# Kernel tuning notes

Hardware: AMD Instinct MI355X
Metric: run time of the kernel (lower is better)

Reference implementation:

```python
import jax, jax.numpy as jnp
import numpy as np

# kernel hyperparameters (base_params)
NUGGET = 0.001
REG_LAMBDA = 0.01
FIT_L, FIT_SIGMA = 1.0, 1.0
MMD_L, MMD_SIGMA = 1.0, 1.0
N, D = 4096, 4


def rbf_gram(X1, X2, l, sigma):
    # [N1,N2] radial kernel: sigma^2 * exp(-||x-x'||^2 / (2 l^2)), vectorized
    sq = (jnp.sum(X1 * X1, axis=1)[:, None]
          + jnp.sum(X2 * X2, axis=1)[None, :]
          - 2.0 * (X1 @ X2.T))
    sq = jnp.maximum(sq, 0.0)
    return (sigma * sigma) * jnp.exp(-sq / (2.0 * l * l))


def setup_inputs() -> dict:
    key = jax.random.key(0)
    kx, ky, kz = jax.random.split(key, 3)
    X = jax.random.normal(kx, (N, D), dtype=jnp.float32)
    Y = jax.random.normal(ky, (N, D), dtype=jnp.float32)
    Z = Y + 0.1 * jax.random.normal(kz, (N, D), dtype=jnp.float32)  # Z init'd from Y, perturbed
    return {"X": X, "Y": Y, "Z": Z}


def reference(X, Y, Z):
    # fit_kXX and its nugget-regularized inverse (precomputed in __init__)
    fit_kXX = rbf_gram(X, X, FIT_L, FIT_SIGMA)
    fit_kXX_inv = jnp.linalg.inv(fit_kXX + NUGGET * jnp.eye(X.shape[0], dtype=X.dtype))

    # loss_fit_z: ||k_ZZ||_F^2 - 2 ||k_ZY||_F^2  (torch matrix norm = Frobenius)
    k_ZZ = rbf_gram(Z, Z, MMD_L, MMD_SIGMA)
    k_ZY = rbf_gram(Z, Y, MMD_L, MMD_SIGMA)
    loss_fit = jnp.sum(k_ZZ * k_ZZ) - 2.0 * jnp.sum(k_ZY * k_ZY)

    # loss_reg_z: reg_lambda * trace(Z^T fit_kXX_inv Z)
    loss_reg = REG_LAMBDA * jnp.sum(Z * (fit_kXX_inv @ Z))

    return loss_fit + loss_reg
```

## Files before the change

### kernel.cpp

```cpp
#include <hip/hip_runtime.h>


#define NN 4096
#define LDA 4100
#define OFF_W   ((size_t)NN*LDA)
#define OFF_ACC (OFF_W + (size_t)NN*4)

__device__ __forceinline__ float rdlane(float v, int l){
    return __int_as_float(__builtin_amdgcn_readlane(__float_as_int(v), l));
}

__device__ void wave_chol64(const float* Dm, float* __restrict__ A, int h){
    const int lane = threadIdx.x & 63;
    float row[64];
#pragma unroll
    for (int q=0;q<16;q++){
        float4 v = *(const float4*)(Dm + lane*68 + q*4);
        row[q*4]=v.x; row[q*4+1]=v.y; row[q*4+2]=v.z; row[q*4+3]=v.w;
    }
#pragma unroll
    for (int j=0;j<64;j++){
        float d  = rdlane(row[j], j);
        float sd = sqrtf(d);
        float inv= 1.0f/sd;
        float v  = (lane==j)? sd : row[j]*inv;
        row[j] = v;
#pragma unroll
        for (int c=j+1;c<64;c++){
            float lc = rdlane(v, c);
            row[c] -= v*lc;
        }
    }
#pragma unroll
    for (int q=0;q<16;q++)
        *(float4*)(A + (size_t)(h+lane)*LDA + h + q*4) =
            make_float4(row[q*4],row[q*4+1],row[q*4+2],row[q*4+3]);
}

__global__ void k_build_A(const float* __restrict__ X, float* __restrict__ A){
    const int i  = blockIdx.y;
    const int j0 = (blockIdx.x*256 + threadIdx.x)*4;
    const float4 xi = *(const float4*)(X + (size_t)i*4);
    float out[4];
#pragma unroll
    for (int s=0;s<4;s++){
        const float4 xj = *(const float4*)(X + (size_t)(j0+s)*4);
        float d0=xi.x-xj.x, d1=xi.y-xj.y, d2=xi.z-xj.z, d3=xi.w-xj.w;
        float sq = d0*d0+d1*d1+d2*d2+d3*d3;
        float v  = __expf(-0.5f*sq);
        if (i == j0+s) v += 0.001f;
        out[s]=v;
    }
    *(float4*)(A + (size_t)i*LDA + j0) = make_float4(out[0],out[1],out[2],out[3]);
}

__global__ void k_init(const float* __restrict__ Z, float* __restrict__ W,
                       double* __restrict__ acc){
    const int i = blockIdx.x*256+threadIdx.x;
    ((float4*)W)[i] = ((const float4*)Z)[i];
    if (blockIdx.x==0 && threadIdx.x==0) acc[0]=0.0;
}

__global__ __launch_bounds__(256) void k_chol0(float* __restrict__ A){
    __shared__ float Dm[64*68];
    const int tid = threadIdx.x;
#pragma unroll
    for (int it=0; it<4; ++it){
        int idx = tid + it*256, r = idx>>4, q = idx&15;
        float4 v = *(const float4*)(A + (size_t)r*LDA + q*4);
        *(float4*)&Dm[r*68 + q*4] = v;
    }
    __syncthreads();
    if (tid < 64) wave_chol64(Dm, A, 0);
}

__global__ __launch_bounds__(256) void k_trsm2(float* __restrict__ A, float* __restrict__ W,
                                               int g){
    __shared__ float Ld[64*68];
    __shared__ float dinv[64];
    const int tid = threadIdx.x;
    const int s0  = g*64;
#pragma unroll
    for (int it=0; it<4; ++it){
        int idx = tid + it*256, r = idx>>4, q = idx&15;
        float4 v = *(const float4*)(A + (size_t)(s0+r)*LDA + s0 + q*4);
        *(float4*)&Ld[r*68 + q*4] = v;
    }
    __syncthreads();
    if (tid < 64) dinv[tid] = 1.0f/Ld[tid*68 + tid];
    __syncthreads();

    const int nRB = (66-g)>>2;
    if ((int)blockIdx.x < nRB){
        const int row = s0 + 64 + blockIdx.x*256 + tid;
        const int rl  = row>4095 ? 4095 : row;
        float x[64];
        const float* src = A + (size_t)rl*LDA + s0;
#pragma unroll
        for (int q=0;q<16;q++){
            float4 v = *(const float4*)(src + q*4);
            x[q*4]=v.x; x[q*4+1]=v.y; x[q*4+2]=v.z; x[q*4+3]=v.w;
        }
#pragma unroll
        for (int c=0;c<64;c++){
            float xc = x[c]*dinv[c];
            x[c] = xc;
#pragma unroll
            for (int t=c+1;t<64;t++) x[t] -= xc*Ld[t*68 + c];
        }
        if (row < 4096){
            float* dst = A + (size_t)row*LDA + s0;
#pragma unroll
            for (int q=0;q<16;q++)
                *(float4*)(dst + q*4) = make_float4(x[q*4],x[q*4+1],x[q*4+2],x[q*4+3]);
        }
    } else {
        if (tid < 64){
            const int lane = tid;
            float4 wv = *(const float4*)(W + (size_t)(s0+lane)*4);
            float w0=wv.x, w1=wv.y, w2=wv.z, w3=wv.w;
#pragma unroll
            for (int j=0;j<64;j++){
                if (lane==j){ float dj=dinv[j]; w0*=dj; w1*=dj; w2*=dj; w3*=dj; }
                float b0=__shfl(w0,j), b1=__shfl(w1,j), b2=__shfl(w2,j), b3=__shfl(w3,j);
                float l = Ld[lane*68 + j];
                if (lane>j){ w0-=l*b0; w1-=l*b1; w2-=l*b2; w3-=l*b3; }
            }
            *(float4*)(W + (size_t)(s0+lane)*4) = make_float4(w0,w1,w2,w3);
        }
    }
}

__global__ __launch_bounds__(256) void k_pupd(float* __restrict__ A, float* __restrict__ W,
                                              int g){
    __shared__ float Sh[2*4352];
    const int tid = threadIdx.x;
    const int g64 = g*64;
    const int i = g&3, ncols = 3-i;
    int idx = blockIdx.x;
    int c_blk=-1, r_blk=-1;
#pragma unroll
    for (int cc=0; cc<3; ++cc){
        if (cc < ncols && c_blk < 0){
            int cb = g+1+cc, cnt = 64-cb;
            if (idx < cnt){ c_blk=cb; r_blk=cb+idx; }
            else idx -= cnt;
        }
    }
    const int tx = tid&15, ty = tid>>4;

    if (c_blk >= 0){
        float* PrT = Sh;
        float* PcT = (r_blk==c_blk) ? Sh : (Sh + 4352);
        const int r0 = r_blk*64, c0 = c_blk*64;
#pragma unroll
        for (int it=0; it<4; ++it){
            int ix = tid + it*256, r = ix>>4, q = ix&15;
            float4 v = *(const float4*)(A + (size_t)(r0+r)*LDA + g64 + q*4);
            PrT[(q*4+0)*68+r]=v.x; PrT[(q*4+1)*68+r]=v.y;
            PrT[(q*4+2)*68+r]=v.z; PrT[(q*4+3)*68+r]=v.w;
        }
        if (r_blk != c_blk){
#pragma unroll
            for (int it=0; it<4; ++it){
                int ix = tid + it*256, r = ix>>4, q = ix&15;
                float4 v = *(const float4*)(A + (size_t)(c0+r)*LDA + g64 + q*4);
                PcT[(q*4+0)*68+r]=v.x; PcT[(q*4+1)*68+r]=v.y;
                PcT[(q*4+2)*68+r]=v.z; PcT[(q*4+3)*68+r]=v.w;
            }
        }
        __syncthreads();
        float acc[4][4]={};
#pragma unroll 8
        for (int t=0;t<64;t++){
            float4 a = *(const float4*)&PrT[t*68 + ty*4];
            float4 b = *(const float4*)&PcT[t*68 + tx*4];
            acc[0][0]+=a.x*b.x; acc[0][1]+=a.x*b.y; acc[0][2]+=a.x*b.z; acc[0][3]+=a.x*b.w;
            acc[1][0]+=a.y*b.x; acc[1][1]+=a.y*b.y; acc[1][2]+=a.y*b.z; acc[1][3]+=a.y*b.w;
            acc[2][0]+=a.z*b.x; acc[2][1]+=a.z*b.y; acc[2][2]+=a.z*b.z; acc[2][3]+=a.z*b.w;
            acc[3][0]+=a.w*b.x; acc[3][1]+=a.w*b.y; acc[3][2]+=a.w*b.z; acc[3][3]+=a.w*b.w;
        }
        if (r_blk==c_blk && c_blk==g+1){
            float* Dm = Sh + 4352;
            __syncthreads();
#pragma unroll
            for (int ii=0;ii<4;ii++){
                float4 c = *(const float4*)(A + (size_t)(r0+ty*4+ii)*LDA + c0 + tx*4);
                c.x-=acc[ii][0]; c.y-=acc[ii][1]; c.z-=acc[ii][2]; c.w-=acc[ii][3];
                *(float4*)&Dm[(ty*4+ii)*68 + tx*4] = c;
            }
            __syncthreads();
            if (tid < 64) wave_chol64(Dm, A, r0);
        } else {
#pragma unroll
            for (int ii=0;ii<4;ii++){
                float* p = A + (size_t)(r0+ty*4+ii)*LDA + c0 + tx*4;
                float4 cv = *(float4*)p;
                cv.x-=acc[ii][0]; cv.y-=acc[ii][1]; cv.z-=acc[ii][2]; cv.w-=acc[ii][3];
                *(float4*)p = cv;
            }
        }
    } else {
        const int wr0 = (g+1+idx)*64;
        float* Lt = Sh;
        float* Ws = Sh + 4352;
#pragma unroll
        for (int it=0; it<4; ++it){
            int ix = tid + it*256, r = ix>>4, q = ix&15;
            float4 v = *(const float4*)(A + (size_t)(wr0+r)*LDA + g64 + q*4);
            *(float4*)&Lt[r*68 + q*4] = v;
        }
        if (tid < 64) *(float4*)&Ws[tid*4] = *(const float4*)(W + (size_t)(g64+tid)*4);
        __syncthreads();
        const int row = tid>>2, cw = tid&3;
        float s = 0.f;
#pragma unroll 16
        for (int t=0;t<64;t++) s += Lt[row*68+t]*Ws[t*4+cw];
        float* wp = W + (size_t)(wr0+row)*4 + cw;
        *wp = *wp - s;
    }
}

__global__ __launch_bounds__(256) void k_upd256(float* __restrict__ A, int S){
    __shared__ float S_[8704];
    const int tid = threadIdx.x;
    const int k0 = S*256, base = k0+256;
    const int T2 = (4096-base)>>7;
    const int nT2 = T2*(T2+1)/2;
    const int tx = tid&15, ty = tid>>4;

    if ((int)blockIdx.x == nT2){
        float* PT = S_;
        float* Dm = S_ + 4352;
        float acc[4][4]={};
        for (int kk=0; kk<4; ++kk){
            __syncthreads();
#pragma unroll
            for (int it=0; it<4; ++it){
                int ix = tid + it*256, r = ix>>4, q = ix&15;
                float4 v = *(const float4*)(A + (size_t)(base+r)*LDA + k0 + kk*64 + q*4);
                PT[(q*4+0)*68+r]=v.x; PT[(q*4+1)*68+r]=v.y;
                PT[(q*4+2)*68+r]=v.z; PT[(q*4+3)*68+r]=v.w;
            }
            __syncthreads();
#pragma unroll 8
            for (int t=0;t<64;t++){
                float4 a = *(const float4*)&PT[t*68 + ty*4];
                float4 b = *(const float4*)&PT[t*68 + tx*4];
                acc[0][0]+=a.x*b.x; acc[0][1]+=a.x*b.y; acc[0][2]+=a.x*b.z; acc[0][3]+=a.x*b.w;
                acc[1][0]+=a.y*b.x; acc[1][1]+=a.y*b.y; acc[1][2]+=a.y*b.z; acc[1][3]+=a.y*b.w;
                acc[2][0]+=a.z*b.x; acc[2][1]+=a.z*b.y; acc[2][2]+=a.z*b.z; acc[2][3]+=a.z*b.w;
                acc[3][0]+=a.w*b.x; acc[3][1]+=a.w*b.y; acc[3][2]+=a.w*b.z; acc[3][3]+=a.w*b.w;
            }
        }
        __syncthreads();
#pragma unroll
        for (int ii=0;ii<4;ii++){
            float4 c = *(const float4*)(A + (size_t)(base+ty*4+ii)*LDA + base + tx*4);
            c.x-=acc[ii][0]; c.y-=acc[ii][1]; c.z-=acc[ii][2]; c.w-=acc[ii][3];
            *(float4*)&Dm[(ty*4+ii)*68 + tx*4] = c;
        }
        __syncthreads();
        if (tid < 64) wave_chol64(Dm, A, base);
        return;
    }

    float* Sa = S_;
    float* Sb = S_ + 4224;
    int t2 = blockIdx.x;
    int bi = (int)((sqrtf(8.f*(float)t2+1.f)-1.f)*0.5f);
    while ((bi+1)*(bi+2)/2 <= t2) ++bi;
    while (bi*(bi+1)/2 > t2) --bi;
    const int bj = t2 - bi*(bi+1)/2;
    const int r0 = base + bi*128, c0 = base + bj*128;
    const bool dg = (bi==bj);
    const float* Sbp = dg ? Sa : Sb;
    int row_[4], q_[4];
#pragma unroll
    for (int it=0;it<4;++it){ int ix=tid+it*256; row_[it]=ix>>3; q_[it]=ix&7; }
    float4 ra[4], rb[4];
#pragma unroll
    for (int it=0;it<4;++it){
        ra[it] = *(const float4*)(A + (size_t)(r0+row_[it])*LDA + k0 + q_[it]*4);
        if (!dg) rb[it] = *(const float4*)(A + (size_t)(c0+row_[it])*LDA + k0 + q_[it]*4);
    }
    float acc[8][8]={};
    for (int kk=0;kk<8;++kk){
        __syncthreads();
#pragma unroll
        for (int it=0;it<4;++it){
            Sa[(q_[it]*4+0)*132+row_[it]]=ra[it].x; Sa[(q_[it]*4+1)*132+row_[it]]=ra[it].y;
            Sa[(q_[it]*4+2)*132+row_[it]]=ra[it].z; Sa[(q_[it]*4+3)*132+row_[it]]=ra[it].w;
            if (!dg){
                Sb[(q_[it]*4+0)*132+row_[it]]=rb[it].x; Sb[(q_[it]*4+1)*132+row_[it]]=rb[it].y;
                Sb[(q_[it]*4+2)*132+row_[it]]=rb[it].z; Sb[(q_[it]*4+3)*132+row_[it]]=rb[it].w;
            }
        }
        __syncthreads();
        if (kk < 7){
            const int kb = k0 + (kk+1)*32;
#pragma unroll
            for (int it=0;it<4;++it){
                ra[it] = *(const float4*)(A + (size_t)(r0+row_[it])*LDA + kb + q_[it]*4);
                if (!dg) rb[it] = *(const float4*)(A + (size_t)(c0+row_[it])*LDA + kb + q_[it]*4);
            }
        }
#pragma unroll 4
        for (int t=0;t<32;++t){
            float4 a0 = *(const float4*)&Sa[t*132 + ty*8];
            float4 a1 = *(const float4*)&Sa[t*132 + ty*8 + 4];
            float4 b0 = *(const float4*)&Sbp[t*132 + tx*8];
            float4 b1 = *(const float4*)&Sbp[t*132 + tx*8 + 4];
            float av[8]={a0.x,a0.y,a0.z,a0.w,a1.x,a1.y,a1.z,a1.w};
            float bv[8]={b0.x,b0.y,b0.z,b0.w,b1.x,b1.y,b1.z,b1.w};
#pragma unroll
            for (int ii=0;ii<8;ii++)
#pragma unroll
                for (int jj=0;jj<8;jj++) acc[ii][jj] += av[ii]*bv[jj];
        }
    }
#pragma unroll
    for (int ii=0;ii<8;ii++){
        const int r = r0 + ty*8 + ii;
        const int c = c0 + tx*8;
        if (r < base+64 && c < base+64) continue;
        float* p = A + (size_t)r*LDA + c;
        float4 c1 = *(float4*)p;
        c1.x-=acc[ii][0]; c1.y-=acc[ii][1]; c1.z-=acc[ii][2]; c1.w-=acc[ii][3];
        *(float4*)p = c1;
        float4 c2 = *(float4*)(p+4);
        c2.x-=acc[ii][4]; c2.y-=acc[ii][5]; c2.z-=acc[ii][6]; c2.w-=acc[ii][7];
        *(float4*)(p+4) = c2;
    }
}

__global__ void k_lossfit(const float* __restrict__ Z, const float* __restrict__ Y,
                          double* __restrict__ acc){
    const int tid=threadIdx.x;
    const int i0=blockIdx.x*8;
    double s=0.0;
    for (int ii=0;ii<8;ii++){
        const float4 zi = *(const float4*)(Z + (size_t)(i0+ii)*4);
        for (int j=tid;j<NN;j+=256){
            float4 zj = *(const float4*)(Z + (size_t)j*4);
            float4 yj = *(const float4*)(Y + (size_t)j*4);
            float d0=zi.x-zj.x, d1=zi.y-zj.y, d2=zi.z-zj.z, d3=zi.w-zj.w;
            float dzz = d0*d0+d1*d1+d2*d2+d3*d3;
            d0=zi.x-yj.x; d1=zi.y-yj.y; d2=zi.z-yj.z; d3=zi.w-yj.w;
            float dzy = d0*d0+d1*d1+d2*d2+d3*d3;
            s += (double)(__expf(-dzz) - 2.f*__expf(-dzy));
        }
    }
    for (int o=32;o;o>>=1) s += __shfl_down(s,o);
    __shared__ double ps[4];
    if ((tid&63)==0) ps[tid>>6]=s;
    __syncthreads();
    if (tid==0) atomicAdd(acc, ps[0]+ps[1]+ps[2]+ps[3]);
}

__global__ void k_finish(const float* __restrict__ W, const double* __restrict__ acc,
                         float* __restrict__ out){
    const int tid=threadIdx.x;
    double s=0.0;
    for (int r=tid;r<NN;r+=256){
        float4 v=*(const float4*)(W+(size_t)r*4);
        s += (double)v.x*v.x+(double)v.y*v.y+(double)v.z*v.z+(double)v.w*v.w;
    }
    for (int o=32;o;o>>=1) s += __shfl_down(s,o);
    __shared__ double ps[4];
    if ((tid&63)==0) ps[tid>>6]=s;
    __syncthreads();
    if (tid==0) out[0] = (float)(acc[0] + 0.01*(ps[0]+ps[1]+ps[2]+ps[3]));
}

extern "C" void kernel_launch(void* const* d_in, const int* in_sizes, int n_in,
                              void* d_out, int out_size, void* d_ws, size_t ws_size,
                              hipStream_t stream){
    const float* X=(const float*)d_in[0];
    const float* Y=(const float*)d_in[1];
    const float* Z=(const float*)d_in[2];
    float* ws   = (float*)d_ws;
    float* A    = ws;
    float* W    = ws + OFF_W;
    double* acc = (double*)(ws + OFF_ACC);

    if (ws_size < (OFF_ACC)*sizeof(float) + 16) return;

    k_init   <<<16,256,0,stream>>>(Z, W, acc);
    k_build_A<<<dim3(NN/1024,NN),256,0,stream>>>(X, A);
    k_lossfit<<<512,256,0,stream>>>(Z, Y, acc);
    k_chol0  <<<1,256,0,stream>>>(A);

    for (int g=0; g<64; ++g){
        const int nRB = (66-g)>>2;
        k_trsm2<<<nRB+1,256,0,stream>>>(A, W, g);
        const int i = g&3, ncols = 3-i;
        int ntile = 0;
        for (int cc=0; cc<ncols; ++cc) ntile += 64-(g+1+cc);
        const int nW = 63-g;
        if (ntile+nW > 0) k_pupd<<<ntile+nW,256,0,stream>>>(A, W, g);
        if (i==3 && g<63){
            const int S = g>>2;
            const int T2 = (4096-(S+1)*256)>>7;
            const int nT2 = T2*(T2+1)/2;
            k_upd256<<<nT2+1,256,0,stream>>>(A, S);
        }
    }
    k_finish<<<1,256,0,stream>>>(W, acc, (float*)d_out);
}
```

Baseline: 3.625 ms.

## Fuse panel TRSM, panel update and forward solve into one launch per step

Replaces the separate trsm and panel-update kernels with one fused kernel per 64-column step. In it, each update block recomputes its own TRSM rows from the diagonal block, the forward substitution on W is folded into the TRSM and Cholesky-solve paths, and the next diagonal block is factored in the same launch. Solved panel rows go to a compact 256-wide Lp buffer, which the 256-step trailing update reads instead of strided A rows. The aim is to halve the number of launches and serial dependencies along the critical path. The cost is redundant triangular solves in every update block, plus a B-tile layout change in the big update kernel.

Result: slower. 4.572 ms (+26.1%).

```diff
diff --git a/kernel.cpp b/kernel.cpp
--- a/kernel.cpp
+++ b/kernel.cpp
@@ -4,13 +4,15 @@
 #define NN 4096
 #define LDA 4100
 #define OFF_W   ((size_t)NN*LDA)
-#define OFF_ACC (OFF_W + (size_t)NN*4)
+#define OFF_LP  (OFF_W + (size_t)NN*4)
+#define OFF_ACC (OFF_LP + (size_t)4096*256)
 
 __device__ __forceinline__ float rdlane(float v, int l){
     return __int_as_float(__builtin_amdgcn_readlane(__float_as_int(v), l));
 }
 
-__device__ void wave_chol64(const float* Dm, float* __restrict__ A, int h){
+__device__ void wave_chol_solve(const float* Dm, float* __restrict__ A, int h,
+                                float4 w, float* __restrict__ W){
     const int lane = threadIdx.x & 63;
     float row[64];
 #pragma unroll
@@ -35,6 +37,15 @@
     for (int q=0;q<16;q++)
         *(float4*)(A + (size_t)(h+lane)*LDA + h + q*4) =
             make_float4(row[q*4],row[q*4+1],row[q*4+2],row[q*4+3]);
+    float w0=w.x,w1=w.y,w2=w.z,w3=w.w;
+#pragma unroll
+    for (int j=0;j<64;j++){
+        if (lane==j){ float dj=1.0f/row[j]; w0*=dj; w1*=dj; w2*=dj; w3*=dj; }
+        float b0=__shfl(w0,j), b1=__shfl(w1,j), b2=__shfl(w2,j), b3=__shfl(w3,j);
+        float l = row[j];
+        if (lane>j){ w0-=l*b0; w1-=l*b1; w2-=l*b2; w3-=l*b3; }
+    }
+    *(float4*)(W + (size_t)(h+lane)*4) = make_float4(w0,w1,w2,w3);
 }
 
 __global__ void k_build_A(const float* __restrict__ X, float* __restrict__ A){
@@ -61,41 +72,50 @@
     if (blockIdx.x==0 && threadIdx.x==0) acc[0]=0.0;
 }
 
-__global__ __launch_bounds__(256) void k_chol0(float* __restrict__ A){
+__global__ __launch_bounds__(256) void k_chol0(float* __restrict__ A, float* __restrict__ W){
     __shared__ float Dm[64*68];
+    const int tid=threadIdx.x;
+#pragma unroll
+    for (int it=0; it<4; ++it){
+        int idx=tid+it*256, r=idx>>4, q=idx&15;
+        *(float4*)&Dm[r*68+q*4] = *(const float4*)(A + (size_t)r*LDA + q*4);
+    }
+    __syncthreads();
+    if (tid<64){
+        float4 w = *(const float4*)(W + (size_t)tid*4);
+        wave_chol_solve(Dm, A, 0, w, W);
+    }
+}
+
+__global__ __launch_bounds__(256) void k_F(float* __restrict__ A, float* __restrict__ W,
+                                           float* __restrict__ Lp, int g){
+    __shared__ float S_[13376];
+    float* Ld   = S_;
+    float* dinv = S_+4352;
+    float* Wg   = S_+4416;
+    float* LrT  = S_+4672;
+    float* LcT  = S_+9024;
     const int tid = threadIdx.x;
-#pragma unroll
+    const int g64 = g*64;
+    const int pend = g|3;
+    const bool hasD = (g&3)!=3;
+    const int nT = (63-g+3)>>2;
+
     for (int it=0; it<4; ++it){
         int idx = tid + it*256, r = idx>>4, q = idx&15;
-        float4 v = *(const float4*)(A + (size_t)r*LDA + q*4);
-        *(float4*)&Dm[r*68 + q*4] = v;
-    }
+        *(float4*)&Ld[r*68+q*4] = *(const float4*)(A + (size_t)(g64+r)*LDA + g64 + q*4);
+    }
+    if (tid < 64) *(float4*)&Wg[tid*4] = *(const float4*)(W + (size_t)(g64+tid)*4);
     __syncthreads();
-    if (tid < 64) wave_chol64(Dm, A, 0);
-}
-
-__global__ __launch_bounds__(256) void k_trsm2(float* __restrict__ A, float* __restrict__ W,
-                                               int g){
-    __shared__ float Ld[64*68];
-    __shared__ float dinv[64];
-    const int tid = threadIdx.x;
-    const int s0  = g*64;
-#pragma unroll
-    for (int it=0; it<4; ++it){
-        int idx = tid + it*256, r = idx>>4, q = idx&15;
-        float4 v = *(const float4*)(A + (size_t)(s0+r)*LDA + s0 + q*4);
-        *(float4*)&Ld[r*68 + q*4] = v;
-    }
+    if (tid < 64) dinv[tid] = 1.0f/Ld[tid*68+tid];
     __syncthreads();
-    if (tid < 64) dinv[tid] = 1.0f/Ld[tid*68 + tid];
-    __syncthreads();
-
-    const int nRB = (66-g)>>2;
-    if ((int)blockIdx.x < nRB){
-        const int row = s0 + 64 + blockIdx.x*256 + tid;
+
+    int bid = blockIdx.x;
+    if (bid < nT){
+        const int row = g64 + 64 + bid*256 + tid;
         const int rl  = row>4095 ? 4095 : row;
         float x[64];
-        const float* src = A + (size_t)rl*LDA + s0;
+        const float* src = A + (size_t)rl*LDA + g64;
 #pragma unroll
         for (int q=0;q<16;q++){
             float4 v = *(const float4*)(src + q*4);
@@ -109,122 +129,143 @@
             for (int t=c+1;t<64;t++) x[t] -= xc*Ld[t*68 + c];
         }
         if (row < 4096){
-            float* dst = A + (size_t)row*LDA + s0;
+            float* lp = Lp + (size_t)row*256 + (g&3)*64;
 #pragma unroll
             for (int q=0;q<16;q++)
-                *(float4*)(dst + q*4) = make_float4(x[q*4],x[q*4+1],x[q*4+2],x[q*4+3]);
-        }
-    } else {
-        if (tid < 64){
-            const int lane = tid;
-            float4 wv = *(const float4*)(W + (size_t)(s0+lane)*4);
-            float w0=wv.x, w1=wv.y, w2=wv.z, w3=wv.w;
-#pragma unroll
-            for (int j=0;j<64;j++){
-                if (lane==j){ float dj=dinv[j]; w0*=dj; w1*=dj; w2*=dj; w3*=dj; }
-                float b0=__shfl(w0,j), b1=__shfl(w1,j), b2=__shfl(w2,j), b3=__shfl(w3,j);
-                float l = Ld[lane*68 + j];
-                if (lane>j){ w0-=l*b0; w1-=l*b1; w2-=l*b2; w3-=l*b3; }
-            }
-            *(float4*)(W + (size_t)(s0+lane)*4) = make_float4(w0,w1,w2,w3);
-        }
-    }
-}
-
-__global__ __launch_bounds__(256) void k_pupd(float* __restrict__ A, float* __restrict__ W,
-                                              int g){
-    __shared__ float Sh[2*4352];
-    const int tid = threadIdx.x;
-    const int g64 = g*64;
-    const int i = g&3, ncols = 3-i;
-    int idx = blockIdx.x;
+                *(float4*)(lp+q*4) = make_float4(x[q*4],x[q*4+1],x[q*4+2],x[q*4+3]);
+            const bool skipW = hasD && ((row>>6) == g+1);
+            if (!skipW){
+                float4 wv = *(const float4*)(W + (size_t)row*4);
+                float s0=0.f,s1=0.f,s2=0.f,s3=0.f;
+#pragma unroll 16
+                for (int t=0;t<64;t++){
+                    float l = x[t];
+                    float4 wg = *(const float4*)&Wg[t*4];
+                    s0 += l*wg.x; s1 += l*wg.y; s2 += l*wg.z; s3 += l*wg.w;
+                }
+                wv.x-=s0; wv.y-=s1; wv.z-=s2; wv.w-=s3;
+                *(float4*)(W + (size_t)row*4) = wv;
+            }
+        }
+        return;
+    }
+    bid -= nT;
+
     int c_blk=-1, r_blk=-1;
-#pragma unroll
-    for (int cc=0; cc<3; ++cc){
-        if (cc < ncols && c_blk < 0){
-            int cb = g+1+cc, cnt = 64-cb;
-            if (idx < cnt){ c_blk=cb; r_blk=cb+idx; }
-            else idx -= cnt;
+    for (int c=g+1; c<=pend; ++c){
+        int st = (c==g+1)? c+1 : c;
+        int cnt = 64-st;
+        if (c_blk<0){
+            if (bid < cnt){ c_blk=c; r_blk=st+bid; }
+            else bid -= cnt;
         }
     }
     const int tx = tid&15, ty = tid>>4;
 
     if (c_blk >= 0){
-        float* PrT = Sh;
-        float* PcT = (r_blk==c_blk) ? Sh : (Sh + 4352);
-        const int r0 = r_blk*64, c0 = c_blk*64;
-#pragma unroll
-        for (int it=0; it<4; ++it){
-            int ix = tid + it*256, r = ix>>4, q = ix&15;
-            float4 v = *(const float4*)(A + (size_t)(r0+r)*LDA + g64 + q*4);
-            PrT[(q*4+0)*68+r]=v.x; PrT[(q*4+1)*68+r]=v.y;
-            PrT[(q*4+2)*68+r]=v.z; PrT[(q*4+3)*68+r]=v.w;
-        }
-        if (r_blk != c_blk){
-#pragma unroll
-            for (int it=0; it<4; ++it){
-                int ix = tid + it*256, r = ix>>4, q = ix&15;
-                float4 v = *(const float4*)(A + (size_t)(c0+r)*LDA + g64 + q*4);
-                PcT[(q*4+0)*68+r]=v.x; PcT[(q*4+1)*68+r]=v.y;
-                PcT[(q*4+2)*68+r]=v.z; PcT[(q*4+3)*68+r]=v.w;
-            }
-        }
-        __syncthreads();
+        const bool dgp = (r_blk==c_blk);
+        const int wv_ = tid>>6, lane = tid&63;
+        if (wv_==0 || (wv_==1 && !dgp)){
+            const int rb  = (wv_==0)? r_blk : c_blk;
+            const int row = rb*64 + lane;
+            float x[64];
+            const float* src = A + (size_t)row*LDA + g64;
+#pragma unroll
+            for (int q=0;q<16;q++){
+                float4 v = *(const float4*)(src + q*4);
+                x[q*4]=v.x; x[q*4+1]=v.y; x[q*4+2]=v.z; x[q*4+3]=v.w;
+            }
+#pragma unroll
+            for (int c=0;c<64;c++){
+                float xc = x[c]*dinv[c];
+                x[c] = xc;
+#pragma unroll
+                for (int t=c+1;t<64;t++) x[t] -= xc*Ld[t*68 + c];
+            }
+            float* dst = (wv_==0)? LrT : LcT;
+#pragma unroll
+            for (int t=0;t<64;t++) dst[t*68+lane] = x[t];
+        }
+        __syncthreads();
+        const float* B = dgp ? LrT : LcT;
         float acc[4][4]={};
 #pragma unroll 8
         for (int t=0;t<64;t++){
-            float4 a = *(const float4*)&PrT[t*68 + ty*4];
-            float4 b = *(const float4*)&PcT[t*68 + tx*4];
+            float4 a = *(const float4*)&LrT[t*68 + ty*4];
+            float4 b = *(const float4*)&B[t*68 + tx*4];
             acc[0][0]+=a.x*b.x; acc[0][1]+=a.x*b.y; acc[0][2]+=a.x*b.z; acc[0][3]+=a.x*b.w;
             acc[1][0]+=a.y*b.x; acc[1][1]+=a.y*b.y; acc[1][2]+=a.y*b.z; acc[1][3]+=a.y*b.w;
             acc[2][0]+=a.z*b.x; acc[2][1]+=a.z*b.y; acc[2][2]+=a.z*b.z; acc[2][3]+=a.z*b.w;
             acc[3][0]+=a.w*b.x; acc[3][1]+=a.w*b.y; acc[3][2]+=a.w*b.z; acc[3][3]+=a.w*b.w;
         }
-        if (r_blk==c_blk && c_blk==g+1){
-            float* Dm = Sh + 4352;
-            __syncthreads();
-#pragma unroll
-            for (int ii=0;ii<4;ii++){
-                float4 c = *(const float4*)(A + (size_t)(r0+ty*4+ii)*LDA + c0 + tx*4);
-                c.x-=acc[ii][0]; c.y-=acc[ii][1]; c.z-=acc[ii][2]; c.w-=acc[ii][3];
-                *(float4*)&Dm[(ty*4+ii)*68 + tx*4] = c;
-            }
-            __syncthreads();
-            if (tid < 64) wave_chol64(Dm, A, r0);
-        } else {
-#pragma unroll
-            for (int ii=0;ii<4;ii++){
-                float* p = A + (size_t)(r0+ty*4+ii)*LDA + c0 + tx*4;
-                float4 cv = *(float4*)p;
-                cv.x-=acc[ii][0]; cv.y-=acc[ii][1]; cv.z-=acc[ii][2]; cv.w-=acc[ii][3];
-                *(float4*)p = cv;
-            }
-        }
-    } else {
-        const int wr0 = (g+1+idx)*64;
-        float* Lt = Sh;
-        float* Ws = Sh + 4352;
-#pragma unroll
-        for (int it=0; it<4; ++it){
-            int ix = tid + it*256, r = ix>>4, q = ix&15;
-            float4 v = *(const float4*)(A + (size_t)(wr0+r)*LDA + g64 + q*4);
-            *(float4*)&Lt[r*68 + q*4] = v;
-        }
-        if (tid < 64) *(float4*)&Ws[tid*4] = *(const float4*)(W + (size_t)(g64+tid)*4);
-        __syncthreads();
-        const int row = tid>>2, cw = tid&3;
-        float s = 0.f;
+        const int r0 = r_blk*64, c0 = c_blk*64;
+#pragma unroll
+        for (int ii=0;ii<4;ii++){
+            float* p = A + (size_t)(r0+ty*4+ii)*LDA + c0 + tx*4;
+            float4 cv = *(float4*)p;
+            cv.x-=acc[ii][0]; cv.y-=acc[ii][1]; cv.z-=acc[ii][2]; cv.w-=acc[ii][3];
+            *(float4*)p = cv;
+        }
+        return;
+    }
+
+    {
+        const int lane = tid&63;
+        const int h = (g+1)*64;
+        if (tid < 64){
+            float x[64];
+            const float* src = A + (size_t)(h+lane)*LDA + g64;
+#pragma unroll
+            for (int q=0;q<16;q++){
+                float4 v = *(const float4*)(src + q*4);
+                x[q*4]=v.x; x[q*4+1]=v.y; x[q*4+2]=v.z; x[q*4+3]=v.w;
+            }
+#pragma unroll
+            for (int c=0;c<64;c++){
+                float xc = x[c]*dinv[c];
+                x[c] = xc;
+#pragma unroll
+                for (int t=c+1;t<64;t++) x[t] -= xc*Ld[t*68 + c];
+            }
+#pragma unroll
+            for (int t=0;t<64;t++) LrT[t*68+lane] = x[t];
+        }
+        __syncthreads();
+        float sacc[4][4]={};
+#pragma unroll 8
+        for (int t=0;t<64;t++){
+            float4 a = *(const float4*)&LrT[t*68 + ty*4];
+            float4 b = *(const float4*)&LrT[t*68 + tx*4];
+            sacc[0][0]+=a.x*b.x; sacc[0][1]+=a.x*b.y; sacc[0][2]+=a.x*b.z; sacc[0][3]+=a.x*b.w;
+            sacc[1][0]+=a.y*b.x; sacc[1][1]+=a.y*b.y; sacc[1][2]+=a.y*b.z; sacc[1][3]+=a.y*b.w;
+            sacc[2][0]+=a.z*b.x; sacc[2][1]+=a.z*b.y; sacc[2][2]+=a.z*b.z; sacc[2][3]+=a.z*b.w;
+            sacc[3][0]+=a.w*b.x; sacc[3][1]+=a.w*b.y; sacc[3][2]+=a.w*b.z; sacc[3][3]+=a.w*b.w;
+        }
+#pragma unroll
+        for (int ii=0;ii<4;ii++){
+            float4 c = *(const float4*)(A + (size_t)(h+ty*4+ii)*LDA + h + tx*4);
+            c.x-=sacc[ii][0]; c.y-=sacc[ii][1]; c.z-=sacc[ii][2]; c.w-=sacc[ii][3];
+            *(float4*)&LcT[(ty*4+ii)*68 + tx*4] = c;
+        }
+        __syncthreads();
+        if (tid < 64){
+            float4 w = *(const float4*)(W + (size_t)(h+lane)*4);
 #pragma unroll 16
-        for (int t=0;t<64;t++) s += Lt[row*68+t]*Ws[t*4+cw];
-        float* wp = W + (size_t)(wr0+row)*4 + cw;
-        *wp = *wp - s;
-    }
-}
-
-__global__ __launch_bounds__(256) void k_upd256(float* __restrict__ A, int S){
+            for (int t=0;t<64;t++){
+                float l = LrT[t*68+lane];
+                float4 wg = *(const float4*)&Wg[t*4];
+                w.x -= l*wg.x; w.y -= l*wg.y; w.z -= l*wg.z; w.w -= l*wg.w;
+            }
+            wave_chol_solve(LcT, A, h, w, W);
+        }
+    }
+}
+
+__global__ __launch_bounds__(256) void k_upd256p(float* __restrict__ A, float* __restrict__ W,
+                                                 const float* __restrict__ Lp, int S){
     __shared__ float S_[8704];
     const int tid = threadIdx.x;
-    const int k0 = S*256, base = k0+256;
+    const int base = S*256 + 256;
     const int T2 = (4096-base)>>7;
     const int nT2 = T2*(T2+1)/2;
     const int tx = tid&15, ty = tid>>4;
@@ -238,7 +279,7 @@
 #pragma unroll
             for (int it=0; it<4; ++it){
                 int ix = tid + it*256, r = ix>>4, q = ix&15;
-                float4 v = *(const float4*)(A + (size_t)(base+r)*LDA + k0 + kk*64 + q*4);
+                float4 v = *(const float4*)(Lp + (size_t)(base+r)*256 + kk*64 + q*4);
                 PT[(q*4+0)*68+r]=v.x; PT[(q*4+1)*68+r]=v.y;
                 PT[(q*4+2)*68+r]=v.z; PT[(q*4+3)*68+r]=v.w;
             }
@@ -261,7 +302,10 @@
             *(float4*)&Dm[(ty*4+ii)*68 + tx*4] = c;
         }
         __syncthreads();
-        if (tid < 64) wave_chol64(Dm, A, base);
+        if (tid < 64){
+            float4 w = *(const float4*)(W + (size_t)(base+tid)*4);
+            wave_chol_solve(Dm, A, base, w, W);
+        }
         return;
     }
 
@@ -281,8 +325,8 @@
     float4 ra[4], rb[4];
 #pragma unroll
     for (int it=0;it<4;++it){
-        ra[it] = *(const float4*)(A + (size_t)(r0+row_[it])*LDA + k0 + q_[it]*4);
-        if (!dg) rb[it] = *(const float4*)(A + (size_t)(c0+row_[it])*LDA + k0 + q_[it]*4);
+        ra[it] = *(const float4*)(Lp + (size_t)(r0+row_[it])*256 + q_[it]*4);
+        if (!dg) rb[it] = *(const float4*)(Lp + (size_t)(c0+row_[it])*256 + q_[it]*4);
     }
     float acc[8][8]={};
     for (int kk=0;kk<8;++kk){
@@ -298,19 +342,19 @@
         }
         __syncthreads();
         if (kk < 7){
-            const int kb = k0 + (kk+1)*32;
+            const int kb = (kk+1)*32;
 #pragma unroll
             for (int it=0;it<4;++it){
-                ra[it] = *(const float4*)(A + (size_t)(r0+row_[it])*LDA + kb + q_[it]*4);
-                if (!dg) rb[it] = *(const float4*)(A + (size_t)(c0+row_[it])*LDA + kb + q_[it]*4);
+                ra[it] = *(const float4*)(Lp + (size_t)(r0+row_[it])*256 + kb + q_[it]*4);
+                if (!dg) rb[it] = *(const float4*)(Lp + (size_t)(c0+row_[it])*256 + kb + q_[it]*4);
             }
         }
 #pragma unroll 4
         for (int t=0;t<32;++t){
             float4 a0 = *(const float4*)&Sa[t*132 + ty*8];
             float4 a1 = *(const float4*)&Sa[t*132 + ty*8 + 4];
-            float4 b0 = *(const float4*)&Sbp[t*132 + tx*8];
-            float4 b1 = *(const float4*)&Sbp[t*132 + tx*8 + 4];
+            float4 b0 = *(const float4*)&Sbp[t*132 + tx*4];
+            float4 b1 = *(const float4*)&Sbp[t*132 + 64 + tx*4];
             float av[8]={a0.x,a0.y,a0.z,a0.w,a1.x,a1.y,a1.z,a1.w};
             float bv[8]={b0.x,b0.y,b0.z,b0.w,b1.x,b1.y,b1.z,b1.w};
 #pragma unroll
@@ -322,15 +366,20 @@
 #pragma unroll
     for (int ii=0;ii<8;ii++){
         const int r = r0 + ty*8 + ii;
-        const int c = c0 + tx*8;
-        if (r < base+64 && c < base+64) continue;
-        float* p = A + (size_t)r*LDA + c;
-        float4 c1 = *(float4*)p;
-        c1.x-=acc[ii][0]; c1.y-=acc[ii][1]; c1.z-=acc[ii][2]; c1.w-=acc[ii][3];
-        *(float4*)p = c1;
-        float4 c2 = *(float4*)(p+4);
-        c2.x-=acc[ii][4]; c2.y-=acc[ii][5]; c2.z-=acc[ii][6]; c2.w-=acc[ii][7];
-        *(float4*)(p+4) = c2;
+        const int c1 = c0 + tx*4;
+        const int c2 = c0 + 64 + tx*4;
+        if (!(r < base+64 && c1 < base+64)){
+            float* p = A + (size_t)r*LDA + c1;
+            float4 cv = *(float4*)p;
+            cv.x-=acc[ii][0]; cv.y-=acc[ii][1]; cv.z-=acc[ii][2]; cv.w-=acc[ii][3];
+            *(float4*)p = cv;
+        }
+        if (!(r < base+64 && c2 < base+64)){
+            float* p = A + (size_t)r*LDA + c2;
+            float4 cv = *(float4*)p;
+            cv.x-=acc[ii][4]; cv.y-=acc[ii][5]; cv.z-=acc[ii][6]; cv.w-=acc[ii][7];
+            *(float4*)p = cv;
+        }
     }
 }
 
@@ -382,28 +431,31 @@
     float* ws   = (float*)d_ws;
     float* A    = ws;
     float* W    = ws + OFF_W;
+    float* Lp   = ws + OFF_LP;
     double* acc = (double*)(ws + OFF_ACC);
 
-    if (ws_size < (OFF_ACC)*sizeof(float) + 16) return;
+    if (ws_size < (OFF_ACC+2)*sizeof(float) + 16) return;
 
     k_init   <<<16,256,0,stream>>>(Z, W, acc);
     k_build_A<<<dim3(NN/1024,NN),256,0,stream>>>(X, A);
     k_lossfit<<<512,256,0,stream>>>(Z, Y, acc);
-    k_chol0  <<<1,256,0,stream>>>(A);
-
-    for (int g=0; g<64; ++g){
-        const int nRB = (66-g)>>2;
-        k_trsm2<<<nRB+1,256,0,stream>>>(A, W, g);
-        const int i = g&3, ncols = 3-i;
-        int ntile = 0;
-        for (int cc=0; cc<ncols; ++cc) ntile += 64-(g+1+cc);
-        const int nW = 63-g;
-        if (ntile+nW > 0) k_pupd<<<ntile+nW,256,0,stream>>>(A, W, g);
-        if (i==3 && g<63){
+    k_chol0  <<<1,256,0,stream>>>(A, W);
+
+    for (int g=0; g<63; ++g){
+        const int nT = (63-g+3)>>2;
+        const int pend = g|3;
+        int nP = 0;
+        for (int c=g+1; c<=pend; ++c){
+            int st = (c==g+1)? c+1 : c;
+            nP += 64-st;
+        }
+        const int hasD = ((g&3)!=3) ? 1 : 0;
+        k_F<<<nT+nP+hasD,256,0,stream>>>(A, W, Lp, g);
+        if ((g&3)==3){
             const int S = g>>2;
             const int T2 = (4096-(S+1)*256)>>7;
             const int nT2 = T2*(T2+1)/2;
-            k_upd256<<<nT2+1,256,0,stream>>>(A, S);
+            k_upd256p<<<nT2+1,256,0,stream>>>(A, W, Lp, S);
         }
     }
     k_finish<<<1,256,0,stream>>>(W, acc, (float*)d_out);
```
